# Performance work log

Hardware: AMD Instinct MI355X
Metric: run time of the kernel (lower is better)

The kernel has to match this reference:

```python
import jax, jax.numpy as jnp
import numpy as np


def setup_inputs() -> dict:
    key = jax.random.key(0)
    kq, kk, kwq, kwk, kwv = jax.random.split(key, 5)
    B, T, C, H = 16, 2048, 1024, 64
    q = jax.random.normal(kq, (B, T, C), dtype=jnp.float32)
    k = jax.random.normal(kk, (B, T, C), dtype=jnp.float32)
    s = 1.0 / np.sqrt(C)
    Wq = jax.random.normal(kwq, (C, H), dtype=jnp.float32) * s
    Wk = jax.random.normal(kwk, (C, H), dtype=jnp.float32) * s
    Wv = jax.random.normal(kwv, (C, H), dtype=jnp.float32) * s
    return {"q": q, "k": k, "Wq": Wq, "Wk": Wk, "Wv": Wv}


def reference(q, k, Wq, Wk, Wv):
    # q, k: (B, T, C); projections are bias-free C -> head_size H
    Q = q @ Wq            # (B, T, H)
    K = k @ Wk            # (B, T, H)
    V = k @ Wv            # (B, T, H)
    T = q.shape[1]
    # NOTE: original scales by input dim C (q.shape[-1]), not head_size
    scale = q.shape[-1] ** (-0.5)
    wei = jnp.einsum('bth,bsh->bts', Q, K) * scale   # (B, T, T)
    causal = jnp.tril(jnp.ones((T, T), dtype=bool))
    wei = jnp.where(causal, wei, -jnp.inf)
    wei = jax.nn.softmax(wei, axis=-1)
    # dropout rate is 0.0 -> identity at inference
    out = jnp.einsum('bts,bsh->bth', wei, V)         # (B, T, H)
    return out
```

## Files before the change

kernel.cpp:

```cpp
#include <hip/hip_runtime.h>
#include <hip/hip_bf16.h>

typedef __bf16 bf16;
typedef __bf16 bf16x8 __attribute__((ext_vector_type(8)));
typedef float f32x4 __attribute__((ext_vector_type(4)));

#define MFMA_16x16x32(A, B, C) __builtin_amdgcn_mfma_f32_16x16x32_bf16(A, B, C, 0, 0, 0)

static_assert(sizeof(bf16x8) == 16, "bf16x8 must be 16B");

__device__ __forceinline__ void gld16(void* lds, const void* g) {
  __builtin_amdgcn_global_load_lds(
      (const __attribute__((address_space(1))) unsigned int*)g,
      (__attribute__((address_space(3))) unsigned int*)lds, 16, 0, 0);
}

__global__ __launch_bounds__(256) void wtrans_kernel(
    const float* __restrict__ Wq, const float* __restrict__ Wk,
    const float* __restrict__ Wv, bf16* __restrict__ Wt)
{
  int idx = blockIdx.x * 256 + threadIdx.x;
  int p = idx >> 16;
  int rem = idx & 65535;
  int h = rem >> 10;
  int c = rem & 1023;
  const float* W = (p == 0) ? Wq : (p == 1) ? Wk : Wv;
  Wt[idx] = (bf16)W[c * 64 + h];
}

__global__ __launch_bounds__(256, 2) void proj_kernel(
    const float* __restrict__ qin, const float* __restrict__ kin,
    const bf16* __restrict__ Wt,
    bf16* __restrict__ Qb, bf16* __restrict__ Kb, bf16* __restrict__ Vtb)
{
  const int p = blockIdx.y;
  const int m0 = blockIdx.x * 128;
  const float* A = (p == 0) ? qin : kin;
  const int nmat = (p == 0) ? 1 : 2;

  __shared__ __align__(16) float As[2][128 * 32];
  __shared__ __align__(16) bf16  Bs[2][2][64 * 32];

  const int tid = threadIdx.x;
  const int lane = tid & 63;
  const int w = tid >> 6;
  const int g = lane >> 4;
  const int r = lane & 15;

  f32x4 acc[2][2][4];
  #pragma unroll
  for (int mt = 0; mt < 2; mt++)
    #pragma unroll
    for (int rf = 0; rf < 2; rf++)
      #pragma unroll
      for (int cf = 0; cf < 4; cf++)
        acc[mt][rf][cf] = (f32x4){0.f, 0.f, 0.f, 0.f};

  const int brow = tid >> 2;
  const int bch = tid & 3;

  auto stage = [&](int buf, int k0) {
    #pragma unroll
    for (int i = 0; i < 4; i++) {
      int ci = i * 256 + tid;
      int row = ci >> 3, ch = ci & 7;
      gld16(&As[buf][ci * 4],
            A + (size_t)(m0 + row) * 1024 + k0 + ch * 4);
    }
    #pragma unroll
    for (int mt = 0; mt < 2; mt++) {
      if (mt < nmat) {
        const bf16* src = Wt + (size_t)((p == 0) ? 0 : 1 + mt) * 65536
                          + (size_t)brow * 1024 + k0 + bch * 8;
        gld16(&Bs[buf][mt][(size_t)tid * 8], src);
      }
    }
  };

  stage(0, 0);

  for (int it = 0; it < 32; ++it) {
    const int cur = it & 1;
    __syncthreads();
    if (it + 1 < 32) stage(cur ^ 1, (it + 1) * 32);

    bf16x8 af[2];
    #pragma unroll
    for (int rf = 0; rf < 2; rf++) {
      const float* ap = &As[cur][(w * 32 + rf * 16 + r) * 32 + g * 8];
      float4 lo = *(const float4*)ap;
      float4 hi = *(const float4*)(ap + 4);
      af[rf] = (bf16x8){(bf16)lo.x, (bf16)lo.y, (bf16)lo.z, (bf16)lo.w,
                        (bf16)hi.x, (bf16)hi.y, (bf16)hi.z, (bf16)hi.w};
    }

    #pragma unroll
    for (int mt = 0; mt < 2; mt++) {
      if (mt < nmat) {
        #pragma unroll
        for (int cf = 0; cf < 4; cf++) {
          bf16x8 bfr = *(const bf16x8*)&Bs[cur][mt][(cf * 16 + r) * 32 + g * 8];
          #pragma unroll
          for (int rf = 0; rf < 2; rf++)
            acc[mt][rf][cf] = MFMA_16x16x32(af[rf], bfr, acc[mt][rf][cf]);
        }
      }
    }
  }

  #pragma unroll
  for (int rf = 0; rf < 2; rf++) {
    #pragma unroll
    for (int cf = 0; cf < 4; cf++) {
      #pragma unroll
      for (int j = 0; j < 4; j++) {
        int rg = m0 + w * 32 + rf * 16 + g * 4 + j;
        int col = cf * 16 + r;
        if (p == 0) {
          Qb[(size_t)rg * 64 + col] = (bf16)acc[0][rf][cf][j];
        } else {
          Kb[(size_t)rg * 64 + col] = (bf16)acc[0][rf][cf][j];
          int bb = rg >> 11, t = rg & 2047;
          Vtb[(size_t)(bb * 64 + col) * 2048 + t] = (bf16)acc[1][rf][cf][j];
        }
      }
    }
  }
}

__global__ __launch_bounds__(256) void attn_kernel(
    const bf16* __restrict__ Qb, const bf16* __restrict__ Kb,
    const bf16* __restrict__ Vtb, float* __restrict__ out)
{
  const int qt = (int)(gridDim.x - 1 - blockIdx.x);
  const int b = blockIdx.y;
  const int tid = threadIdx.x;
  const int lane = tid & 63;
  const int w = tid >> 6;
  const int g = lane >> 4;
  const int r = lane & 15;

  __shared__ __align__(16) bf16 Ks[64][80];
  __shared__ __align__(16) bf16 Vs[64][80];
  __shared__ __align__(16) bf16 Ps[4][16][80];

  const int q0 = qt * 64 + w * 16;
  const bf16* qp = Qb + (size_t)(b * 2048 + q0 + r) * 64 + g * 8;
  const bf16x8 qf0 = *(const bf16x8*)qp;
  const bf16x8 qf1 = *(const bf16x8*)(qp + 32);

  f32x4 acc_o[4];
  #pragma unroll
  for (int hf = 0; hf < 4; hf++) acc_o[hf] = (f32x4){0.f, 0.f, 0.f, 0.f};
  float m_r[4] = {-1e30f, -1e30f, -1e30f, -1e30f};
  float l_r[4] = {0.f, 0.f, 0.f, 0.f};
  const float scale = 0.03125f;

  const int sh = tid >> 2;
  const int sc = (tid & 3) * 16;

  for (int kv = 0; kv <= qt; kv++) {
    {
      const bf16* kp = Kb + (size_t)(b * 2048 + kv * 64 + sh) * 64 + sc;
      *(bf16x8*)&Ks[sh][sc]     = *(const bf16x8*)kp;
      *(bf16x8*)&Ks[sh][sc + 8] = *(const bf16x8*)(kp + 8);
      const bf16* vp = Vtb + (size_t)(b * 64 + sh) * 2048 + kv * 64 + sc;
      *(bf16x8*)&Vs[sh][sc]     = *(const bf16x8*)vp;
      *(bf16x8*)&Vs[sh][sc + 8] = *(const bf16x8*)(vp + 8);
    }
    __syncthreads();

    f32x4 s[4];
    #pragma unroll
    for (int cf = 0; cf < 4; cf++) {
      bf16x8 kf0 = *(const bf16x8*)&Ks[cf * 16 + r][g * 8];
      bf16x8 kf1 = *(const bf16x8*)&Ks[cf * 16 + r][32 + g * 8];
      f32x4 t = (f32x4){0.f, 0.f, 0.f, 0.f};
      t = MFMA_16x16x32(qf0, kf0, t);
      t = MFMA_16x16x32(qf1, kf1, t);
      s[cf] = t;
    }

    const bool diag = (kv == qt);
    float pm[4] = {-1e30f, -1e30f, -1e30f, -1e30f};
    #pragma unroll
    for (int cf = 0; cf < 4; cf++) {
      #pragma unroll
      for (int j = 0; j < 4; j++) {
        float v = s[cf][j] * scale;
        if (diag && (cf * 16 + r) > (w * 16 + g * 4 + j)) v = -1e30f;
        s[cf][j] = v;
        pm[j] = fmaxf(pm[j], v);
      }
    }
    #pragma unroll
    for (int j = 0; j < 4; j++) {
      #pragma unroll
      for (int msk = 1; msk < 16; msk <<= 1)
        pm[j] = fmaxf(pm[j], __shfl_xor(pm[j], msk, 64));
    }
    float corr[4];
    #pragma unroll
    for (int j = 0; j < 4; j++) {
      float mn = fmaxf(m_r[j], pm[j]);
      corr[j] = __expf(m_r[j] - mn);
      m_r[j] = mn;
    }
    float rs[4] = {0.f, 0.f, 0.f, 0.f};
    #pragma unroll
    for (int cf = 0; cf < 4; cf++) {
      #pragma unroll
      for (int j = 0; j < 4; j++) {
        float pv = __expf(s[cf][j] - m_r[j]);
        s[cf][j] = pv;
        rs[j] += pv;
      }
    }
    #pragma unroll
    for (int j = 0; j < 4; j++) {
      #pragma unroll
      for (int msk = 1; msk < 16; msk <<= 1)
        rs[j] += __shfl_xor(rs[j], msk, 64);
      l_r[j] = l_r[j] * corr[j] + rs[j];
    }
    #pragma unroll
    for (int hf = 0; hf < 4; hf++)
      #pragma unroll
      for (int j = 0; j < 4; j++)
        acc_o[hf][j] *= corr[j];

    #pragma unroll
    for (int cf = 0; cf < 4; cf++)
      #pragma unroll
      for (int j = 0; j < 4; j++)
        Ps[w][g * 4 + j][cf * 16 + r] = (bf16)s[cf][j];

    __syncthreads();

    #pragma unroll
    for (int ss = 0; ss < 2; ss++) {
      bf16x8 pf = *(const bf16x8*)&Ps[w][r][ss * 32 + g * 8];
      #pragma unroll
      for (int hf = 0; hf < 4; hf++) {
        bf16x8 vf = *(const bf16x8*)&Vs[hf * 16 + r][ss * 32 + g * 8];
        acc_o[hf] = MFMA_16x16x32(pf, vf, acc_o[hf]);
      }
    }
    __syncthreads();
  }

  float inv[4];
  #pragma unroll
  for (int j = 0; j < 4; j++) inv[j] = 1.0f / l_r[j];
  const size_t ob = (size_t)(b * 2048 + q0) * 64;
  #pragma unroll
  for (int hf = 0; hf < 4; hf++)
    #pragma unroll
    for (int j = 0; j < 4; j++)
      out[ob + (size_t)(g * 4 + j) * 64 + hf * 16 + r] = acc_o[hf][j] * inv[j];
}

extern "C" void kernel_launch(void* const* d_in, const int* in_sizes, int n_in,
                              void* d_out, int out_size, void* d_ws, size_t ws_size,
                              hipStream_t stream)
{
  const float* q  = (const float*)d_in[0];
  const float* k  = (const float*)d_in[1];
  const float* Wq = (const float*)d_in[2];
  const float* Wk = (const float*)d_in[3];
  const float* Wv = (const float*)d_in[4];
  float* out = (float*)d_out;

  char* ws = (char*)d_ws;
  bf16* Qb  = (bf16*)(ws);
  bf16* Kb  = (bf16*)(ws + (4u << 20));
  bf16* Vtb = (bf16*)(ws + (8u << 20));
  bf16* Wt  = (bf16*)(ws + (12u << 20));

  hipLaunchKernelGGL(wtrans_kernel, dim3(768), dim3(256), 0, stream,
                     Wq, Wk, Wv, Wt);
  hipLaunchKernelGGL(proj_kernel, dim3(256, 2), dim3(256), 0, stream,
                     q, k, Wt, Qb, Kb, Vtb);
  hipLaunchKernelGGL(attn_kernel, dim3(32, 16), dim3(256), 0, stream,
                     Qb, Kb, Vtb, out);
}
```

Before: 127.9 us.

## Triple-buffer projection GEMM loads and swizzle LDS layouts to avoid bank conflicts

The projection kernel moves from double to triple buffering of the A and W tiles. Waits now use explicit vmcnt counters with raw s_barrier, so up to two future k-chunks stay in flight while one is computed. The LDS layouts of the fp32 A tile and the bf16 W tile are XOR-swizzled to reduce bank conflicts on the fragment reads. The cost is more LDS per block (three buffers) and hand-written waitcnt logic that depends on exactly six loads per stage.

```diff
diff --git a/kernel.cpp b/kernel.cpp
--- a/kernel.cpp
+++ b/kernel.cpp
@@ -37,9 +37,11 @@
   const int m0 = blockIdx.x * 128;
   const float* A = (p == 0) ? qin : kin;
   const int nmat = (p == 0) ? 1 : 2;
-
-  __shared__ __align__(16) float As[2][128 * 32];
-  __shared__ __align__(16) bf16  Bs[2][2][64 * 32];
+  const int mat0 = (p == 0) ? 0 : 1;
+  const int mat1 = (p == 0) ? 0 : 2;
+
+  __shared__ __align__(16) float As[3][128 * 32];
+  __shared__ __align__(16) bf16  Bs[3][2][64 * 32];
 
   const int tid = threadIdx.x;
   const int lane = tid & 63;
@@ -56,57 +58,67 @@
       for (int cf = 0; cf < 4; cf++)
         acc[mt][rf][cf] = (f32x4){0.f, 0.f, 0.f, 0.f};
 
-  const int brow = tid >> 2;
-  const int bch = tid & 3;
-
   auto stage = [&](int buf, int k0) {
     #pragma unroll
     for (int i = 0; i < 4; i++) {
       int ci = i * 256 + tid;
-      int row = ci >> 3, ch = ci & 7;
+      int row = ci >> 3, pch = ci & 7;
       gld16(&As[buf][ci * 4],
-            A + (size_t)(m0 + row) * 1024 + k0 + ch * 4);
-    }
-    #pragma unroll
-    for (int mt = 0; mt < 2; mt++) {
-      if (mt < nmat) {
-        const bf16* src = Wt + (size_t)((p == 0) ? 0 : 1 + mt) * 65536
-                          + (size_t)brow * 1024 + k0 + bch * 8;
-        gld16(&Bs[buf][mt][(size_t)tid * 8], src);
-      }
+            A + (size_t)(m0 + row) * 1024 + k0 + ((pch ^ (row & 7)) << 2));
+    }
+    {
+      int brow = tid >> 2, bch = tid & 3;
+      int lch = bch ^ ((brow >> 1) & 3);
+      const bf16* s0 = Wt + (size_t)mat0 * 65536 + (size_t)brow * 1024 + k0 + (lch << 3);
+      const bf16* s1 = Wt + (size_t)mat1 * 65536 + (size_t)brow * 1024 + k0 + (lch << 3);
+      gld16(&Bs[buf][0][tid * 8], s0);
+      gld16(&Bs[buf][1][tid * 8], s1);
     }
   };
 
-  stage(0, 0);
-
-  for (int it = 0; it < 32; ++it) {
-    const int cur = it & 1;
-    __syncthreads();
-    if (it + 1 < 32) stage(cur ^ 1, (it + 1) * 32);
-
+  auto compute = [&](int cur) {
     bf16x8 af[2];
     #pragma unroll
     for (int rf = 0; rf < 2; rf++) {
-      const float* ap = &As[cur][(w * 32 + rf * 16 + r) * 32 + g * 8];
-      float4 lo = *(const float4*)ap;
-      float4 hi = *(const float4*)(ap + 4);
+      int arow = w * 32 + rf * 16 + r;
+      const float* base = &As[cur][arow * 32];
+      float4 lo = *(const float4*)(base + ((( 2 * g )     ^ (arow & 7)) << 2));
+      float4 hi = *(const float4*)(base + ((( 2 * g + 1 ) ^ (arow & 7)) << 2));
       af[rf] = (bf16x8){(bf16)lo.x, (bf16)lo.y, (bf16)lo.z, (bf16)lo.w,
                         (bf16)hi.x, (bf16)hi.y, (bf16)hi.z, (bf16)hi.w};
     }
-
     #pragma unroll
     for (int mt = 0; mt < 2; mt++) {
       if (mt < nmat) {
         #pragma unroll
         for (int cf = 0; cf < 4; cf++) {
-          bf16x8 bfr = *(const bf16x8*)&Bs[cur][mt][(cf * 16 + r) * 32 + g * 8];
+          int hrow = cf * 16 + r;
+          bf16x8 bfr = *(const bf16x8*)
+              &Bs[cur][mt][hrow * 32 + ((g ^ ((hrow >> 1) & 3)) << 3)];
           #pragma unroll
           for (int rf = 0; rf < 2; rf++)
             acc[mt][rf][cf] = MFMA_16x16x32(af[rf], bfr, acc[mt][rf][cf]);
         }
       }
     }
+  };
+
+  stage(0, 0);
+  stage(1, 32);
+  stage(2, 64);
+
+  int cur = 0;
+  for (int it = 0; it < 30; ++it) {
+    asm volatile("s_waitcnt vmcnt(12)\n\ts_barrier" ::: "memory");
+    compute(cur);
+    asm volatile("s_waitcnt lgkmcnt(0)\n\ts_barrier" ::: "memory");
+    if (it < 29) stage(cur, (it + 3) * 32);
+    cur = (cur == 2) ? 0 : cur + 1;
   }
+  asm volatile("s_waitcnt vmcnt(6)\n\ts_barrier" ::: "memory");
+  compute(0);
+  asm volatile("s_waitcnt vmcnt(0)\n\ts_barrier" ::: "memory");
+  compute(1);
 
   #pragma unroll
   for (int rf = 0; rf < 2; rf++) {
```

After: 127.9 us. No clear change (-0.0%).
